# Optimization experiments

Measured on AMD Instinct MI355X. Metric: run time of the kernel, lower is better.

The kernel has to match this reference:

```python
import jax, jax.numpy as jnp
import numpy as np

B, S, D = 1, 4096, 2048
H = 16
HD = D // H  # 128
BASE = 10000.0


def setup_inputs() -> dict:
    key = jax.random.key(0)
    ks = jax.random.split(key, 6)
    hidden_states = jax.random.normal(ks[0], (B, S, D), dtype=jnp.float32)
    position_ids = jnp.broadcast_to(jnp.arange(S, dtype=jnp.int64 if jax.config.jax_enable_x64 else jnp.int32), (B, S))
    scale = 1.0 / np.sqrt(D)
    Wq = jax.random.normal(ks[1], (D, D), dtype=jnp.float32) * scale
    Wk = jax.random.normal(ks[2], (D, D), dtype=jnp.float32) * scale
    Wv = jax.random.normal(ks[3], (D, D), dtype=jnp.float32) * scale
    Wo = jax.random.normal(ks[4], (D, D), dtype=jnp.float32) * scale
    return {"hidden_states": hidden_states, "Wq": Wq, "Wk": Wk, "Wv": Wv, "Wo": Wo, "position_ids": position_ids}


def _rotate_half(x):
    x1, x2 = x[..., : x.shape[-1] // 2], x[..., x.shape[-1] // 2 :]
    return jnp.concatenate((-x2, x1), axis=-1)


def reference(hidden_states, Wq, Wk, Wv, Wo, position_ids):
    # QKV projections (torch Linear: x @ W.T)
    q = hidden_states @ Wq.T  # [B,S,D]
    k = hidden_states @ Wk.T
    v = hidden_states @ Wv.T
    # split heads -> [B,H,S,HD]
    q = q.reshape(B, S, H, HD).transpose(0, 2, 1, 3)
    k = k.reshape(B, S, H, HD).transpose(0, 2, 1, 3)
    v = v.reshape(B, S, H, HD).transpose(0, 2, 1, 3)
    # RoPE tables over seq positions
    inv_freq = 1.0 / (BASE ** (jnp.arange(0, HD, 2, dtype=jnp.float32) / HD))  # [HD/2]
    t = jnp.arange(S, dtype=jnp.float32)
    freqs = t[:, None] * inv_freq[None, :]            # [S, HD/2]
    emb = jnp.concatenate((freqs, freqs), axis=-1)    # [S, HD]
    cos = jnp.cos(emb)[position_ids][:, None]         # [B,1,S,HD]
    sin = jnp.sin(emb)[position_ids][:, None]
    q = q * cos + _rotate_half(q) * sin
    k = k * cos + _rotate_half(k) * sin
    # attention (num_kv_heads == num_heads, so no GQA repeat)
    scores = jnp.einsum("bhqd,bhkd->bhqk", q, k) / jnp.sqrt(jnp.float32(HD))
    attn = jax.nn.softmax(scores, axis=-1)
    out = jnp.einsum("bhqk,bhkd->bhqd", attn, v)      # [B,H,S,HD]
    out = out.transpose(0, 2, 1, 3).reshape(B, S, D)
    return out @ Wo.T
```

## Files before the change

kernel.cpp:

```cpp
#include <hip/hip_runtime.h>
#include <hip/hip_bf16.h>

#define S_LEN 4096
#define DMODEL 2048
#define NHEADS 16
#define HEADDIM 128
#define LDQ 6144

typedef __attribute__((ext_vector_type(8))) short bf16x8;
typedef __attribute__((ext_vector_type(4))) float f32x4;

__device__ __forceinline__ float bf2f(ushort u) {
  union { unsigned int i; float f; } x; x.i = ((unsigned int)u) << 16; return x.f;
}
__device__ __forceinline__ ushort f2bf(float f) {
  union { float f; unsigned int i; } x; x.f = f;
  unsigned int u = x.i;
  unsigned int r = u + 0x7fffu + ((u >> 16) & 1u);
  return (ushort)(r >> 16);
}
__device__ __forceinline__ unsigned int cvtpk(float a, float b) {
  unsigned int r;
  asm("v_cvt_pk_bf16_f32 %0, %1, %2" : "=v"(r) : "v"(a), "v"(b));
  return r;
}
__device__ __forceinline__ float fexp2(float x) {
  float r;
  asm("v_exp_f32 %0, %1" : "=v"(r) : "v"(x));
  return r;
}

__device__ __forceinline__ void gload16(const ushort* g, ushort* l) {
  __builtin_amdgcn_global_load_lds(
      (const __attribute__((address_space(1))) unsigned int*)g,
      (__attribute__((address_space(3))) unsigned int*)l, 16, 0, 0);
}

__global__ __launch_bounds__(256) void rope_table_kernel(float* __restrict__ cosT,
                                                         float* __restrict__ sinT) {
  int idx = blockIdx.x * 256 + threadIdx.x;
  int t = idx >> 6, j = idx & 63;
  float expo = (float)(2 * j) / 128.0f;
  float inv = 1.0f / powf(10000.0f, expo);
  float f = (float)t * inv;
  cosT[idx] = cosf(f);
  sinT[idx] = sinf(f);
}

__global__ __launch_bounds__(256) void convert_kernel(const float* __restrict__ in,
                                                      ushort* __restrict__ hi) {
  int i = (blockIdx.x * 256 + threadIdx.x) * 4;
  float4 v = *reinterpret_cast<const float4*>(&in[i]);
  ushort4 h;
  h.x = f2bf(v.x); h.y = f2bf(v.y); h.z = f2bf(v.z); h.w = f2bf(v.w);
  *reinterpret_cast<ushort4*>(&hi[i]) = h;
}

__global__ __launch_bounds__(256) void prep_weights(const float* __restrict__ Wq,
                                                    const float* __restrict__ Wk,
                                                    const float* __restrict__ Wv,
                                                    const float* __restrict__ Wo,
                                                    ushort* __restrict__ Wqkv,
                                                    ushort* __restrict__ Woh) {
  int i = (blockIdx.x * 256 + threadIdx.x) * 4;
  int which = blockIdx.y;
  const float* src = (which == 0) ? Wq : (which == 1) ? Wk : (which == 2) ? Wv : Wo;
  ushort* dst = (which == 3) ? Woh : (Wqkv + (size_t)which * DMODEL * DMODEL);
  float4 v = *reinterpret_cast<const float4*>(&src[i]);
  ushort4 h;
  h.x = f2bf(v.x); h.y = f2bf(v.y); h.z = f2bf(v.z); h.w = f2bf(v.w);
  *reinterpret_cast<ushort4*>(&dst[i]) = h;
}

__global__ __launch_bounds__(256) void gemm_qkv(const ushort* __restrict__ Ah_,
                                                const ushort* __restrict__ Bh_,
                                                ushort* __restrict__ Cout,
                                                int M, int N, int K) {
  __shared__ __align__(16) ushort sAh[128 * 64], sBh[128 * 64];
  const int tid = threadIdx.x;
  const int wave = tid >> 6, lane = tid & 63;
  const int lg = lane >> 4, lm = lane & 15;
  const int nwg = gridDim.x * gridDim.y;
  const int id = blockIdx.y * gridDim.x + blockIdx.x;
  const int cpx = nwg >> 3;
  const int swz = (id & 7) * cpx + (id >> 3);
  const int nbx = N >> 7;
  const int m0 = (swz / nbx) * 128, n0 = (swz % nbx) * 128;
  const int wm = (wave >> 1) * 64, wn = (wave & 1) * 64;
  f32x4 acc[4][4] = {};

  int srow[4], scc[4], lbs[4];
#pragma unroll
  for (int it = 0; it < 4; ++it) {
    int ci = it * 256 + wave * 64 + lane;
    srow[it] = ci >> 3;
    scc[it] = (ci & 7) ^ (srow[it] & 7);
    lbs[it] = (it * 256 + wave * 64) * 8;
  }

  for (int k0 = 0; k0 < K; k0 += 64) {
    __syncthreads();
#pragma unroll
    for (int it = 0; it < 4; ++it) {
      size_t ga = (size_t)(m0 + srow[it]) * K + k0 + scc[it] * 8;
      size_t gb = (size_t)(n0 + srow[it]) * K + k0 + scc[it] * 8;
      gload16(&Ah_[ga], &sAh[lbs[it]]);
      gload16(&Bh_[gb], &sBh[lbs[it]]);
    }
    __syncthreads();
    bf16x8 ah[4][2], bh[4][2];
#pragma unroll
    for (int t = 0; t < 4; ++t)
#pragma unroll
      for (int kc = 0; kc < 2; ++kc) {
        int Ra = wm + t * 16 + lm;
        int Rb = wn + t * 16 + lm;
        int pa_ = ((kc * 4 + lg) ^ (Ra & 7)) * 8;
        int pb_ = ((kc * 4 + lg) ^ (Rb & 7)) * 8;
        ah[t][kc] = *reinterpret_cast<const bf16x8*>(&sAh[Ra * 64 + pa_]);
        bh[t][kc] = *reinterpret_cast<const bf16x8*>(&sBh[Rb * 64 + pb_]);
      }
#pragma unroll
    for (int kc = 0; kc < 2; ++kc)
#pragma unroll
      for (int mi = 0; mi < 4; ++mi)
#pragma unroll
        for (int ni = 0; ni < 4; ++ni)
          acc[mi][ni] = __builtin_amdgcn_mfma_f32_16x16x32_bf16(ah[mi][kc], bh[ni][kc], acc[mi][ni], 0, 0, 0);
  }
#pragma unroll
  for (int mi = 0; mi < 4; ++mi)
#pragma unroll
    for (int ni = 0; ni < 4; ++ni)
#pragma unroll
      for (int j = 0; j < 4; ++j) {
        int row = m0 + wm + mi * 16 + lg * 4 + j;
        int col = n0 + wn + ni * 16 + lm;
        Cout[(size_t)row * N + col] = f2bf(acc[mi][ni][j]);
      }
}

__global__ __launch_bounds__(256) void gemm1o64(const ushort* __restrict__ Ah_,
                                                const ushort* __restrict__ Bh_,
                                                float* __restrict__ Cout,
                                                int M, int N, int K) {
  __shared__ __align__(16) ushort sAh[128 * 64], sBh[128 * 64];
  const int tid = threadIdx.x;
  const int wave = tid >> 6, lane = tid & 63;
  const int lg = lane >> 4, lm = lane & 15;
  const int nwg = gridDim.x * gridDim.y;
  const int id = blockIdx.y * gridDim.x + blockIdx.x;
  const int cpx = nwg >> 3;
  const int swz = (id & 7) * cpx + (id >> 3);
  const int nbx = N >> 7;
  const int m0 = (swz / nbx) * 128, n0 = (swz % nbx) * 128;
  const int wm = (wave >> 1) * 64, wn = (wave & 1) * 64;
  f32x4 acc[4][4] = {};

  int srow[4], scc[4], lbs[4];
#pragma unroll
  for (int it = 0; it < 4; ++it) {
    int ci = it * 256 + wave * 64 + lane;
    srow[it] = ci >> 3;
    scc[it] = (ci & 7) ^ (srow[it] & 7);
    lbs[it] = (it * 256 + wave * 64) * 8;
  }

  for (int k0 = 0; k0 < K; k0 += 64) {
    __syncthreads();
#pragma unroll
    for (int it = 0; it < 4; ++it) {
      size_t ga = (size_t)(m0 + srow[it]) * K + k0 + scc[it] * 8;
      size_t gb = (size_t)(n0 + srow[it]) * K + k0 + scc[it] * 8;
      gload16(&Ah_[ga], &sAh[lbs[it]]);
      gload16(&Bh_[gb], &sBh[lbs[it]]);
    }
    __syncthreads();
    bf16x8 ah[4][2], bh[4][2];
#pragma unroll
    for (int t = 0; t < 4; ++t)
#pragma unroll
      for (int kc = 0; kc < 2; ++kc) {
        int Ra = wm + t * 16 + lm;
        int Rb = wn + t * 16 + lm;
        int pa_ = ((kc * 4 + lg) ^ (Ra & 7)) * 8;
        int pb_ = ((kc * 4 + lg) ^ (Rb & 7)) * 8;
        ah[t][kc] = *reinterpret_cast<const bf16x8*>(&sAh[Ra * 64 + pa_]);
        bh[t][kc] = *reinterpret_cast<const bf16x8*>(&sBh[Rb * 64 + pb_]);
      }
#pragma unroll
    for (int kc = 0; kc < 2; ++kc)
#pragma unroll
      for (int mi = 0; mi < 4; ++mi)
#pragma unroll
        for (int ni = 0; ni < 4; ++ni)
          acc[mi][ni] = __builtin_amdgcn_mfma_f32_16x16x32_bf16(ah[mi][kc], bh[ni][kc], acc[mi][ni], 0, 0, 0);
  }
#pragma unroll
  for (int mi = 0; mi < 4; ++mi)
#pragma unroll
    for (int ni = 0; ni < 4; ++ni)
#pragma unroll
      for (int j = 0; j < 4; ++j) {
        int row = m0 + wm + mi * 16 + lg * 4 + j;
        int col = n0 + wn + ni * 16 + lm;
        Cout[(size_t)row * N + col] = acc[mi][ni][j];
      }
}

__global__ __launch_bounds__(256) void rope2_kernel(ushort* __restrict__ QKV,
                                                    const int* __restrict__ pos,
                                                    const float* __restrict__ cosT,
                                                    const float* __restrict__ sinT) {
  int t = blockIdx.x * 256 + threadIdx.x;
  int j0 = (t & 7) * 8;
  int hh = (t >> 3) & 15;
  int s = t >> 7;
  int p = pos[s];
  float cs[8], sn[8];
  *reinterpret_cast<float4*>(&cs[0]) = *reinterpret_cast<const float4*>(&cosT[p * 64 + j0]);
  *reinterpret_cast<float4*>(&cs[4]) = *reinterpret_cast<const float4*>(&cosT[p * 64 + j0 + 4]);
  *reinterpret_cast<float4*>(&sn[0]) = *reinterpret_cast<const float4*>(&sinT[p * 64 + j0]);
  *reinterpret_cast<float4*>(&sn[4]) = *reinterpret_cast<const float4*>(&sinT[p * 64 + j0 + 4]);
  size_t base = (size_t)s * LDQ + hh * HEADDIM + j0;
  union u8 { uint4 v; ushort e[8]; };
  u8 qa, qb, ka, kb;
  qa.v = *reinterpret_cast<const uint4*>(&QKV[base]);
  qb.v = *reinterpret_cast<const uint4*>(&QKV[base + 64]);
  ka.v = *reinterpret_cast<const uint4*>(&QKV[base + DMODEL]);
  kb.v = *reinterpret_cast<const uint4*>(&QKV[base + DMODEL + 64]);
  const float scl = 0.12751742f;
#pragma unroll
  for (int e = 0; e < 8; ++e) {
    float q1 = bf2f(qa.e[e]), q2 = bf2f(qb.e[e]);
    float k1 = bf2f(ka.e[e]), k2 = bf2f(kb.e[e]);
    qa.e[e] = f2bf((q1 * cs[e] - q2 * sn[e]) * scl);
    qb.e[e] = f2bf((q2 * cs[e] + q1 * sn[e]) * scl);
    ka.e[e] = f2bf(k1 * cs[e] - k2 * sn[e]);
    kb.e[e] = f2bf(k2 * cs[e] + k1 * sn[e]);
  }
  *reinterpret_cast<uint4*>(&QKV[base]) = qa.v;
  *reinterpret_cast<uint4*>(&QKV[base + 64]) = qb.v;
  *reinterpret_cast<uint4*>(&QKV[base + DMODEL]) = ka.v;
  *reinterpret_cast<uint4*>(&QKV[base + DMODEL + 64]) = kb.v;
}

__global__ __launch_bounds__(256) void transpose_kernel(const ushort* __restrict__ Vr,
                                                        ushort* __restrict__ Vt) {
  __shared__ __align__(16) ushort tile[64 * 72];
  int tid = threadIdx.x;
  int s0 = blockIdx.x * 64, c0 = blockIdx.y * 64;
#pragma unroll
  for (int it = 0; it < 2; ++it) {
    int i = tid + it * 256;
    int r = i >> 3, c = i & 7;
    *reinterpret_cast<uint4*>(&tile[r * 72 + c * 8]) =
        *reinterpret_cast<const uint4*>(&Vr[(size_t)(s0 + r) * LDQ + c0 + c * 8]);
  }
  __syncthreads();
#pragma unroll
  for (int it = 0; it < 2; ++it) {
    int i = tid + it * 256;
    int cr = i >> 3, sc = i & 7;
    ushort tmp[8];
#pragma unroll
    for (int j = 0; j < 8; ++j) tmp[j] = tile[(sc * 8 + j) * 72 + cr];
    *reinterpret_cast<uint4*>(&Vt[(size_t)(c0 + cr) * S_LEN + s0 + sc * 8]) =
        *reinterpret_cast<uint4*>(tmp);
  }
}

#define FTILE(STC, STN, VCUR, KWB, VWB, KRB, T)                                           \
  {                                                                                       \
    float m16[2];                                                                         \
    _Pragma("unroll") for (int t2 = 0; t2 < 2; ++t2) {                                    \
      float m = fmaxf(STC[t2][0][0], STC[t2][0][1]);                                      \
      m = fmaxf(fmaxf(m, STC[t2][0][2]), STC[t2][0][3]);                                  \
      m = fmaxf(fmaxf(m, STC[t2][1][0]), STC[t2][1][1]);                                  \
      m = fmaxf(fmaxf(m, STC[t2][1][2]), STC[t2][1][3]);                                  \
      m = fmaxf(fmaxf(m, STC[t2][2][0]), STC[t2][2][1]);                                  \
      m = fmaxf(fmaxf(m, STC[t2][2][2]), STC[t2][2][3]);                                  \
      m = fmaxf(fmaxf(m, STC[t2][3][0]), STC[t2][3][1]);                                  \
      m = fmaxf(fmaxf(m, STC[t2][3][2]), STC[t2][3][3]);                                  \
      m = fmaxf(m, __shfl_xor(m, 16));                                                    \
      m = fmaxf(m, __shfl_xor(m, 32));                                                    \
      m16[t2] = m;                                                                        \
    }                                                                                     \
    bool grow = (m16[0] > mrun[0] + 11.5f) || (m16[1] > mrun[1] + 11.5f);                 \
    if (__any(grow)) {                                                                    \
      _Pragma("unroll") for (int t2 = 0; t2 < 2; ++t2) {                                  \
        float mn = fmaxf(mrun[t2], m16[t2]);                                              \
        float scl = fexp2(mrun[t2] - mn);                                                 \
        mrun[t2] = mn;                                                                    \
        float sj[4];                                                                      \
        _Pragma("unroll") for (int j = 0; j < 4; ++j) sj[j] = __shfl(scl, lg * 4 + j);    \
        _Pragma("unroll") for (int j = 0; j < 4; ++j) osum[t2][j] *= sj[j];               \
        _Pragma("unroll") for (int nb = 0; nb < 8; ++nb)                                  \
            _Pragma("unroll") for (int j = 0; j < 4; ++j) oacc[t2][nb][j] *= sj[j];       \
      }                                                                                   \
    }                                                                                     \
    _Pragma("unroll") for (int t2 = 0; t2 < 2; ++t2)                                      \
        _Pragma("unroll") for (int nf = 0; nf < 4; ++nf)                                  \
            _Pragma("unroll") for (int j = 0; j < 4; ++j)                                 \
                STC[t2][nf][j] = fexp2(STC[t2][nf][j] - mrun[t2]);                        \
    bf16x8 pa[2][2];                                                                      \
    _Pragma("unroll") for (int t2 = 0; t2 < 2; ++t2)                                      \
        _Pragma("unroll") for (int kk = 0; kk < 2; ++kk) {                                \
      union { unsigned int u[4]; bf16x8 v; } w_;                                          \
      w_.u[0] = cvtpk(STC[t2][kk][0], STC[t2][kk][1]);                                    \
      w_.u[1] = cvtpk(STC[t2][kk][2], STC[t2][kk][3]);                                    \
      w_.u[2] = cvtpk(STC[t2][2 + kk][0], STC[t2][2 + kk][1]);                            \
      w_.u[3] = cvtpk(STC[t2][2 + kk][2], STC[t2][2 + kk][3]);                            \
      pa[t2][kk] = w_.v;                                                                  \
    }                                                                                     \
    __builtin_amdgcn_s_setprio(1);                                                        \
    _Pragma("unroll") for (int t2 = 0; t2 < 2; ++t2) {                                    \
      osum[t2] = __builtin_amdgcn_mfma_f32_16x16x32_bf16(pa[t2][0], ones, osum[t2], 0, 0, 0); \
      osum[t2] = __builtin_amdgcn_mfma_f32_16x16x32_bf16(pa[t2][1], ones, osum[t2], 0, 0, 0); \
    }                                                                                     \
    _Pragma("unroll") for (int nb = 0; nb < 8; ++nb)                                      \
        _Pragma("unroll") for (int kk = 0; kk < 2; ++kk) {                                \
      int pc = (kk * 4 + lg) ^ (lm & 7);                                                  \
      bf16x8 vfrag = *reinterpret_cast<const bf16x8*>(&VCUR[(nb * 16 + lm) * 64 + pc * 8]); \
      oacc[0][nb] = __builtin_amdgcn_mfma_f32_16x16x32_bf16(pa[0][kk], vfrag, oacc[0][nb], 0, 0, 0); \
      oacc[1][nb] = __builtin_amdgcn_mfma_f32_16x16x32_bf16(pa[1][kk], vfrag, oacc[1][nb], 0, 0, 0); \
    }                                                                                     \
    __builtin_amdgcn_s_setprio(0);                                                        \
    __syncthreads();                                                                      \
    if ((T) + 2 < 64) {                                                                   \
      const size_t ko_ = (size_t)((T) + 2) * 64;                                          \
      _Pragma("unroll") for (int k = 0; k < 4; ++k) {                                     \
        gload16(pK[k] + ko_ * LDQ, &KWB[lbs[k]]);                                         \
        gload16(pV[k] + ko_, &VWB[lbs[k]]);                                               \
      }                                                                                   \
    }                                                                                     \
    if ((T) + 1 < 64) {                                                                   \
      _Pragma("unroll") for (int t2 = 0; t2 < 2; ++t2)                                    \
          _Pragma("unroll") for (int nf = 0; nf < 4; ++nf) STN[t2][nf] = fzero;           \
      __builtin_amdgcn_s_setprio(1);                                                      \
      _Pragma("unroll") for (int nf = 0; nf < 4; ++nf)                                    \
          _Pragma("unroll") for (int kc = 0; kc < 4; ++kc) {                              \
        int pc = (kc * 4 + lg) ^ (lm & 7);                                                \
        bf16x8 kfrag = *reinterpret_cast<const bf16x8*>(&KRB[(nf * 16 + lm) * 128 + pc * 8]); \
        STN[0][nf] = __builtin_amdgcn_mfma_f32_16x16x32_bf16(kfrag, qh[0][kc], STN[0][nf], 0, 0, 0); \
        STN[1][nf] = __builtin_amdgcn_mfma_f32_16x16x32_bf16(kfrag, qh[1][kc], STN[1][nf], 0, 0, 0); \
      }                                                                                   \
      __builtin_amdgcn_s_setprio(0);                                                      \
    }                                                                                     \
  }

__global__ __launch_bounds__(256, 2) void flash14_kernel(const ushort* __restrict__ QKV,
                                                         const ushort* __restrict__ Vt,
                                                         ushort* __restrict__ Oh) {
  __shared__ __align__(16) ushort KtA[64 * 128];
  __shared__ __align__(16) ushort KtB[64 * 128];
  __shared__ __align__(16) ushort VsA[128 * 64];
  __shared__ __align__(16) ushort VsB[128 * 64];
  const int tid = threadIdx.x;
  const int wave = tid >> 6, lane = tid & 63;
  const int lg = lane >> 4, lm = lane & 15;
  const int id = blockIdx.y * gridDim.x + blockIdx.x;
  const int o = (id & 7) * 64 + (id >> 3);
  const int h = o >> 5;
  const int q0 = (o & 31) * 128;
  const f32x4 fzero = {};

  bf16x8 qh[2][4];
#pragma unroll
  for (int t2 = 0; t2 < 2; ++t2) {
    int qrow = q0 + wave * 32 + t2 * 16 + lm;
#pragma unroll
    for (int kc = 0; kc < 4; ++kc)
      qh[t2][kc] = *reinterpret_cast<const bf16x8*>(
          &QKV[(size_t)qrow * LDQ + h * HEADDIM + kc * 32 + lg * 8]);
  }

  bf16x8 ones;
#pragma unroll
  for (int i = 0; i < 8; ++i) ones[i] = (short)0x3f80;

  auto rho = [](int s) {
    return 32 * ((s >> 4) & 1) + 8 * ((s >> 2) & 3) + 4 * (s >> 5) + (s & 3);
  };
  const ushort* Kb = QKV + DMODEL;
  const ushort* pK[4];
  const ushort* pV[4];
  int lbs[4];
#pragma unroll
  for (int k = 0; k < 4; ++k) {
    int ci = k * 256 + wave * 64 + lane;
    int ks = ci >> 4;
    int kcc = (ci & 15) ^ (ks & 7);
    pK[k] = Kb + (size_t)rho(ks) * LDQ + h * HEADDIM + kcc * 8;
    int vd = ci >> 3;
    int vcc = (ci & 7) ^ (vd & 7);
    pV[k] = Vt + (size_t)(h * HEADDIM + vd) * S_LEN + vcc * 8;
    lbs[k] = (k * 256 + wave * 64) * 8;
  }

  f32x4 oacc[2][8] = {};
  f32x4 osum[2] = {};
  float mrun[2];
#pragma unroll
  for (int t2 = 0; t2 < 2; ++t2) mrun[t2] = -3.0e38f;

#pragma unroll
  for (int k = 0; k < 4; ++k) {
    gload16(pK[k], &KtA[lbs[k]]);
    gload16(pV[k], &VsA[lbs[k]]);
  }
  __syncthreads();
#pragma unroll
  for (int k = 0; k < 4; ++k) {
    gload16(pK[k] + (size_t)64 * LDQ, &KtB[lbs[k]]);
    gload16(pV[k] + 64, &VsB[lbs[k]]);
  }
  f32x4 stA[2][4], stB[2][4];
#pragma unroll
  for (int t2 = 0; t2 < 2; ++t2)
#pragma unroll
    for (int nf = 0; nf < 4; ++nf) stA[t2][nf] = fzero;
  __builtin_amdgcn_s_setprio(1);
#pragma unroll
  for (int nf = 0; nf < 4; ++nf)
#pragma unroll
    for (int kc = 0; kc < 4; ++kc) {
      int pc = (kc * 4 + lg) ^ (lm & 7);
      bf16x8 kfrag = *reinterpret_cast<const bf16x8*>(&KtA[(nf * 16 + lm) * 128 + pc * 8]);
      stA[0][nf] = __builtin_amdgcn_mfma_f32_16x16x32_bf16(kfrag, qh[0][kc], stA[0][nf], 0, 0, 0);
      stA[1][nf] = __builtin_amdgcn_mfma_f32_16x16x32_bf16(kfrag, qh[1][kc], stA[1][nf], 0, 0, 0);
    }
  __builtin_amdgcn_s_setprio(0);

  for (int tp = 0; tp < 32; ++tp) {
    const int t0 = 2 * tp;
    FTILE(stA, stB, VsA, KtA, VsA, KtB, t0)
    FTILE(stB, stA, VsB, KtB, VsB, KtA, t0 + 1)
  }

#pragma unroll
  for (int t2 = 0; t2 < 2; ++t2) {
    float linv[4];
#pragma unroll
    for (int j = 0; j < 4; ++j) linv[j] = 1.0f / osum[t2][j];
#pragma unroll
    for (int nb = 0; nb < 8; ++nb)
#pragma unroll
      for (int j = 0; j < 4; ++j) {
        int row = q0 + wave * 32 + t2 * 16 + lg * 4 + j;
        int col = h * HEADDIM + nb * 16 + lm;
        Oh[(size_t)row * DMODEL + col] = f2bf(oacc[t2][nb][j] * linv[j]);
      }
  }
}

extern "C" void kernel_launch(void* const* d_in, const int* in_sizes, int n_in,
                              void* d_out, int out_size, void* d_ws, size_t ws_size,
                              hipStream_t stream) {
  (void)in_sizes; (void)n_in; (void)out_size; (void)ws_size;
  const float* X  = (const float*)d_in[0];
  const float* Wq = (const float*)d_in[1];
  const float* Wk = (const float*)d_in[2];
  const float* Wv = (const float*)d_in[3];
  const float* Wo = (const float*)d_in[4];
  const int* pos  = (const int*)d_in[5];
  float* out = (float*)d_out;

  ushort* wb = (ushort*)d_ws;
  const size_t SD = (size_t)S_LEN * DMODEL;
  const size_t DD = (size_t)DMODEL * DMODEL;

  ushort* Xh   = wb;
  ushort* QKV  = wb + 2 * SD;
  ushort* Vt   = wb + 5 * SD;
  ushort* W0h  = wb + 6 * SD;
  ushort* Wqkv = wb + 7 * SD;
  float* cosT  = (float*)(wb + 9 * SD);
  float* sinT  = cosT + (size_t)S_LEN * 64;
  ushort* OhB  = Wqkv;

  rope_table_kernel<<<S_LEN * 64 / 256, 256, 0, stream>>>(cosT, sinT);
  convert_kernel<<<SD / 1024, 256, 0, stream>>>(X, Xh);
  prep_weights<<<dim3(DD / 1024, 4), 256, 0, stream>>>(Wq, Wk, Wv, Wo, Wqkv, W0h);

  gemm_qkv<<<dim3(LDQ / 128, S_LEN / 128), 256, 0, stream>>>(Xh, Wqkv, QKV, S_LEN, LDQ, DMODEL);

  rope2_kernel<<<(S_LEN * 1024 / 8) / 256, 256, 0, stream>>>(QKV, pos, cosT, sinT);
  transpose_kernel<<<dim3(S_LEN / 64, DMODEL / 64), 256, 0, stream>>>(QKV + 2 * DMODEL, Vt);

  flash14_kernel<<<dim3(32, 16), 256, 0, stream>>>(QKV, Vt, OhB);

  dim3 gemmGrid(DMODEL / 128, S_LEN / 128);
  gemm1o64<<<gemmGrid, 256, 0, stream>>>(OhB, W0h, out, S_LEN, DMODEL, DMODEL);
}
```

Before: 339.9 us.

## Software-pipeline flash attention QK^T one tile ahead; fuse prep kernels

Restructures the flash attention loop so each iteration computes QK^T for the next K tile before running softmax and PV on the previous scores. This lets the MFMA work overlap with the exp/softmax VALU work, and K and V loads are now issued on separate schedules into their buffers. The three preprocessing kernels (rope table, X conversion, weight conversion) are also merged into one launch with a 7-row grid to cut launch overhead. The cost is more live registers for the two score tiles and more intricate buffer-reuse timing.

```diff
diff --git a/kernel.cpp b/kernel.cpp
--- a/kernel.cpp
+++ b/kernel.cpp
@@ -36,40 +36,41 @@
       (__attribute__((address_space(3))) unsigned int*)l, 16, 0, 0);
 }
 
-__global__ __launch_bounds__(256) void rope_table_kernel(float* __restrict__ cosT,
-                                                         float* __restrict__ sinT) {
-  int idx = blockIdx.x * 256 + threadIdx.x;
-  int t = idx >> 6, j = idx & 63;
-  float expo = (float)(2 * j) / 128.0f;
-  float inv = 1.0f / powf(10000.0f, expo);
-  float f = (float)t * inv;
-  cosT[idx] = cosf(f);
-  sinT[idx] = sinf(f);
-}
-
-__global__ __launch_bounds__(256) void convert_kernel(const float* __restrict__ in,
-                                                      ushort* __restrict__ hi) {
-  int i = (blockIdx.x * 256 + threadIdx.x) * 4;
-  float4 v = *reinterpret_cast<const float4*>(&in[i]);
-  ushort4 h;
-  h.x = f2bf(v.x); h.y = f2bf(v.y); h.z = f2bf(v.z); h.w = f2bf(v.w);
-  *reinterpret_cast<ushort4*>(&hi[i]) = h;
-}
-
-__global__ __launch_bounds__(256) void prep_weights(const float* __restrict__ Wq,
-                                                    const float* __restrict__ Wk,
-                                                    const float* __restrict__ Wv,
-                                                    const float* __restrict__ Wo,
-                                                    ushort* __restrict__ Wqkv,
-                                                    ushort* __restrict__ Woh) {
-  int i = (blockIdx.x * 256 + threadIdx.x) * 4;
+__global__ __launch_bounds__(256) void prep_all(const float* __restrict__ X,
+                                                const float* __restrict__ Wq,
+                                                const float* __restrict__ Wk,
+                                                const float* __restrict__ Wv,
+                                                const float* __restrict__ Wo,
+                                                ushort* __restrict__ Xh,
+                                                ushort* __restrict__ Wqkv,
+                                                ushort* __restrict__ Woh,
+                                                float* __restrict__ cosT,
+                                                float* __restrict__ sinT) {
   int which = blockIdx.y;
-  const float* src = (which == 0) ? Wq : (which == 1) ? Wk : (which == 2) ? Wv : Wo;
-  ushort* dst = (which == 3) ? Woh : (Wqkv + (size_t)which * DMODEL * DMODEL);
-  float4 v = *reinterpret_cast<const float4*>(&src[i]);
-  ushort4 h;
-  h.x = f2bf(v.x); h.y = f2bf(v.y); h.z = f2bf(v.z); h.w = f2bf(v.w);
-  *reinterpret_cast<ushort4*>(&dst[i]) = h;
+  if (which < 4) {
+    int i = (blockIdx.x * 256 + threadIdx.x) * 4;
+    const float* src = (which == 0) ? Wq : (which == 1) ? Wk : (which == 2) ? Wv : Wo;
+    ushort* dst = (which == 3) ? Woh : (Wqkv + (size_t)which * DMODEL * DMODEL);
+    float4 v = *reinterpret_cast<const float4*>(&src[i]);
+    ushort4 h;
+    h.x = f2bf(v.x); h.y = f2bf(v.y); h.z = f2bf(v.z); h.w = f2bf(v.w);
+    *reinterpret_cast<ushort4*>(&dst[i]) = h;
+  } else if (which < 6) {
+    int i = (((which - 4) * 4096 + blockIdx.x) * 256 + threadIdx.x) * 4;
+    float4 v = *reinterpret_cast<const float4*>(&X[i]);
+    ushort4 h;
+    h.x = f2bf(v.x); h.y = f2bf(v.y); h.z = f2bf(v.z); h.w = f2bf(v.w);
+    *reinterpret_cast<ushort4*>(&Xh[i]) = h;
+  } else {
+    if (blockIdx.x >= 1024) return;
+    int idx = blockIdx.x * 256 + threadIdx.x;
+    int t = idx >> 6, j = idx & 63;
+    float expo = (float)(2 * j) / 128.0f;
+    float inv = 1.0f / powf(10000.0f, expo);
+    float f = (float)t * inv;
+    cosT[idx] = cosf(f);
+    sinT[idx] = sinf(f);
+  }
 }
 
 __global__ __launch_bounds__(256) void gemm_qkv(const ushort* __restrict__ Ah_,
@@ -270,18 +271,34 @@
   }
 }
 
-#define FTILE(STC, STN, VCUR, KWB, VWB, KRB, T)                                           \
+
+#define QKT15(STC, KRD)                                                                   \
+  {                                                                                       \
+    _Pragma("unroll") for (int t2 = 0; t2 < 2; ++t2)                                      \
+        _Pragma("unroll") for (int nf = 0; nf < 4; ++nf) STC[t2][nf] = fzero;             \
+    __builtin_amdgcn_s_setprio(1);                                                        \
+    _Pragma("unroll") for (int nf = 0; nf < 4; ++nf)                                      \
+        _Pragma("unroll") for (int kc = 0; kc < 4; ++kc) {                                \
+      int pc = (kc * 4 + lg) ^ (lm & 7);                                                  \
+      bf16x8 kfrag = *reinterpret_cast<const bf16x8*>(&KRD[(nf * 16 + lm) * 128 + pc * 8]); \
+      STC[0][nf] = __builtin_amdgcn_mfma_f32_16x16x32_bf16(kfrag, qh[0][kc], STC[0][nf], 0, 0, 0); \
+      STC[1][nf] = __builtin_amdgcn_mfma_f32_16x16x32_bf16(kfrag, qh[1][kc], STC[1][nf], 0, 0, 0); \
+    }                                                                                     \
+    __builtin_amdgcn_s_setprio(0);                                                        \
+  }
+
+#define SMPV15(STP, VPR)                                                                  \
   {                                                                                       \
     float m16[2];                                                                         \
     _Pragma("unroll") for (int t2 = 0; t2 < 2; ++t2) {                                    \
-      float m = fmaxf(STC[t2][0][0], STC[t2][0][1]);                                      \
-      m = fmaxf(fmaxf(m, STC[t2][0][2]), STC[t2][0][3]);                                  \
-      m = fmaxf(fmaxf(m, STC[t2][1][0]), STC[t2][1][1]);                                  \
-      m = fmaxf(fmaxf(m, STC[t2][1][2]), STC[t2][1][3]);                                  \
-      m = fmaxf(fmaxf(m, STC[t2][2][0]), STC[t2][2][1]);                                  \
-      m = fmaxf(fmaxf(m, STC[t2][2][2]), STC[t2][2][3]);                                  \
-      m = fmaxf(fmaxf(m, STC[t2][3][0]), STC[t2][3][1]);                                  \
-      m = fmaxf(fmaxf(m, STC[t2][3][2]), STC[t2][3][3]);                                  \
+      float m = fmaxf(STP[t2][0][0], STP[t2][0][1]);                                      \
+      m = fmaxf(fmaxf(m, STP[t2][0][2]), STP[t2][0][3]);                                  \
+      m = fmaxf(fmaxf(m, STP[t2][1][0]), STP[t2][1][1]);                                  \
+      m = fmaxf(fmaxf(m, STP[t2][1][2]), STP[t2][1][3]);                                  \
+      m = fmaxf(fmaxf(m, STP[t2][2][0]), STP[t2][2][1]);                                  \
+      m = fmaxf(fmaxf(m, STP[t2][2][2]), STP[t2][2][3]);                                  \
+      m = fmaxf(fmaxf(m, STP[t2][3][0]), STP[t2][3][1]);                                  \
+      m = fmaxf(fmaxf(m, STP[t2][3][2]), STP[t2][3][3]);                                  \
       m = fmaxf(m, __shfl_xor(m, 16));                                                    \
       m = fmaxf(m, __shfl_xor(m, 32));                                                    \
       m16[t2] = m;                                                                        \
@@ -302,15 +319,15 @@
     _Pragma("unroll") for (int t2 = 0; t2 < 2; ++t2)                                      \
         _Pragma("unroll") for (int nf = 0; nf < 4; ++nf)                                  \
             _Pragma("unroll") for (int j = 0; j < 4; ++j)                                 \
-                STC[t2][nf][j] = fexp2(STC[t2][nf][j] - mrun[t2]);                        \
+                STP[t2][nf][j] = fexp2(STP[t2][nf][j] - mrun[t2]);                        \
     bf16x8 pa[2][2];                                                                      \
     _Pragma("unroll") for (int t2 = 0; t2 < 2; ++t2)                                      \
         _Pragma("unroll") for (int kk = 0; kk < 2; ++kk) {                                \
       union { unsigned int u[4]; bf16x8 v; } w_;                                          \
-      w_.u[0] = cvtpk(STC[t2][kk][0], STC[t2][kk][1]);                                    \
-      w_.u[1] = cvtpk(STC[t2][kk][2], STC[t2][kk][3]);                                    \
-      w_.u[2] = cvtpk(STC[t2][2 + kk][0], STC[t2][2 + kk][1]);                            \
-      w_.u[3] = cvtpk(STC[t2][2 + kk][2], STC[t2][2 + kk][3]);                            \
+      w_.u[0] = cvtpk(STP[t2][kk][0], STP[t2][kk][1]);                                    \
+      w_.u[1] = cvtpk(STP[t2][kk][2], STP[t2][kk][3]);                                    \
+      w_.u[2] = cvtpk(STP[t2][2 + kk][0], STP[t2][2 + kk][1]);                            \
+      w_.u[3] = cvtpk(STP[t2][2 + kk][2], STP[t2][2 + kk][3]);                            \
       pa[t2][kk] = w_.v;                                                                  \
     }                                                                                     \
     __builtin_amdgcn_s_setprio(1);                                                        \
@@ -321,35 +338,29 @@
     _Pragma("unroll") for (int nb = 0; nb < 8; ++nb)                                      \
         _Pragma("unroll") for (int kk = 0; kk < 2; ++kk) {                                \
       int pc = (kk * 4 + lg) ^ (lm & 7);                                                  \
-      bf16x8 vfrag = *reinterpret_cast<const bf16x8*>(&VCUR[(nb * 16 + lm) * 64 + pc * 8]); \
+      bf16x8 vfrag = *reinterpret_cast<const bf16x8*>(&VPR[(nb * 16 + lm) * 64 + pc * 8]); \
       oacc[0][nb] = __builtin_amdgcn_mfma_f32_16x16x32_bf16(pa[0][kk], vfrag, oacc[0][nb], 0, 0, 0); \
       oacc[1][nb] = __builtin_amdgcn_mfma_f32_16x16x32_bf16(pa[1][kk], vfrag, oacc[1][nb], 0, 0, 0); \
     }                                                                                     \
     __builtin_amdgcn_s_setprio(0);                                                        \
+  }
+
+#define BODY15(STC, STP, KRD, VPR, T)                                                     \
+  {                                                                                       \
+    QKT15(STC, KRD)                                                                       \
+    SMPV15(STP, VPR)                                                                      \
     __syncthreads();                                                                      \
     if ((T) + 2 < 64) {                                                                   \
       const size_t ko_ = (size_t)((T) + 2) * 64;                                          \
-      _Pragma("unroll") for (int k = 0; k < 4; ++k) {                                     \
-        gload16(pK[k] + ko_ * LDQ, &KWB[lbs[k]]);                                         \
-        gload16(pV[k] + ko_, &VWB[lbs[k]]);                                               \
-      }                                                                                   \
+      _Pragma("unroll") for (int k = 0; k < 4; ++k) gload16(pK[k] + ko_ * LDQ, &KRD[lbs[k]]); \
     }                                                                                     \
     if ((T) + 1 < 64) {                                                                   \
-      _Pragma("unroll") for (int t2 = 0; t2 < 2; ++t2)                                    \
-          _Pragma("unroll") for (int nf = 0; nf < 4; ++nf) STN[t2][nf] = fzero;           \
-      __builtin_amdgcn_s_setprio(1);                                                      \
-      _Pragma("unroll") for (int nf = 0; nf < 4; ++nf)                                    \
-          _Pragma("unroll") for (int kc = 0; kc < 4; ++kc) {                              \
-        int pc = (kc * 4 + lg) ^ (lm & 7);                                                \
-        bf16x8 kfrag = *reinterpret_cast<const bf16x8*>(&KRB[(nf * 16 + lm) * 128 + pc * 8]); \
-        STN[0][nf] = __builtin_amdgcn_mfma_f32_16x16x32_bf16(kfrag, qh[0][kc], STN[0][nf], 0, 0, 0); \
-        STN[1][nf] = __builtin_amdgcn_mfma_f32_16x16x32_bf16(kfrag, qh[1][kc], STN[1][nf], 0, 0, 0); \
-      }                                                                                   \
-      __builtin_amdgcn_s_setprio(0);                                                      \
-    }                                                                                     \
-  }
-
-__global__ __launch_bounds__(256, 2) void flash14_kernel(const ushort* __restrict__ QKV,
+      const size_t vo_ = (size_t)((T) + 1) * 64;                                          \
+      _Pragma("unroll") for (int k = 0; k < 4; ++k) gload16(pV[k] + vo_, &VPR[lbs[k]]);   \
+    }                                                                                     \
+  }
+
+__global__ __launch_bounds__(256, 2) void flash15_kernel(const ushort* __restrict__ QKV,
                                                          const ushort* __restrict__ Vt,
                                                          ushort* __restrict__ Oh) {
   __shared__ __align__(16) ushort KtA[64 * 128];
@@ -404,6 +415,8 @@
 #pragma unroll
   for (int t2 = 0; t2 < 2; ++t2) mrun[t2] = -3.0e38f;
 
+  f32x4 stA[2][4], stB[2][4];
+
 #pragma unroll
   for (int k = 0; k < 4; ++k) {
     gload16(pK[k], &KtA[lbs[k]]);
@@ -411,32 +424,24 @@
   }
   __syncthreads();
 #pragma unroll
+  for (int k = 0; k < 4; ++k) gload16(pK[k] + (size_t)64 * LDQ, &KtB[lbs[k]]);
+
+  QKT15(stA, KtA)
+  __syncthreads();
+#pragma unroll
   for (int k = 0; k < 4; ++k) {
-    gload16(pK[k] + (size_t)64 * LDQ, &KtB[lbs[k]]);
+    gload16(pK[k] + (size_t)128 * LDQ, &KtA[lbs[k]]);
     gload16(pV[k] + 64, &VsB[lbs[k]]);
   }
-  f32x4 stA[2][4], stB[2][4];
-#pragma unroll
-  for (int t2 = 0; t2 < 2; ++t2)
-#pragma unroll
-    for (int nf = 0; nf < 4; ++nf) stA[t2][nf] = fzero;
-  __builtin_amdgcn_s_setprio(1);
-#pragma unroll
-  for (int nf = 0; nf < 4; ++nf)
-#pragma unroll
-    for (int kc = 0; kc < 4; ++kc) {
-      int pc = (kc * 4 + lg) ^ (lm & 7);
-      bf16x8 kfrag = *reinterpret_cast<const bf16x8*>(&KtA[(nf * 16 + lm) * 128 + pc * 8]);
-      stA[0][nf] = __builtin_amdgcn_mfma_f32_16x16x32_bf16(kfrag, qh[0][kc], stA[0][nf], 0, 0, 0);
-      stA[1][nf] = __builtin_amdgcn_mfma_f32_16x16x32_bf16(kfrag, qh[1][kc], stA[1][nf], 0, 0, 0);
-    }
-  __builtin_amdgcn_s_setprio(0);
-
-  for (int tp = 0; tp < 32; ++tp) {
-    const int t0 = 2 * tp;
-    FTILE(stA, stB, VsA, KtA, VsA, KtB, t0)
-    FTILE(stB, stA, VsB, KtB, VsB, KtA, t0 + 1)
-  }
+
+  for (int tp = 0; tp < 31; ++tp) {
+    const int t1 = 2 * tp + 1;
+    BODY15(stB, stA, KtB, VsA, t1)
+    BODY15(stA, stB, KtA, VsB, t1 + 1)
+  }
+  BODY15(stB, stA, KtB, VsA, 63)
+
+  SMPV15(stB, VsB)
 
 #pragma unroll
   for (int t2 = 0; t2 < 2; ++t2) {
@@ -479,16 +484,14 @@
   float* sinT  = cosT + (size_t)S_LEN * 64;
   ushort* OhB  = Wqkv;
 
-  rope_table_kernel<<<S_LEN * 64 / 256, 256, 0, stream>>>(cosT, sinT);
-  convert_kernel<<<SD / 1024, 256, 0, stream>>>(X, Xh);
-  prep_weights<<<dim3(DD / 1024, 4), 256, 0, stream>>>(Wq, Wk, Wv, Wo, Wqkv, W0h);
+  prep_all<<<dim3(DD / 1024, 7), 256, 0, stream>>>(X, Wq, Wk, Wv, Wo, Xh, Wqkv, W0h, cosT, sinT);
 
   gemm_qkv<<<dim3(LDQ / 128, S_LEN / 128), 256, 0, stream>>>(Xh, Wqkv, QKV, S_LEN, LDQ, DMODEL);
 
   rope2_kernel<<<(S_LEN * 1024 / 8) / 256, 256, 0, stream>>>(QKV, pos, cosT, sinT);
   transpose_kernel<<<dim3(S_LEN / 64, DMODEL / 64), 256, 0, stream>>>(QKV + 2 * DMODEL, Vt);
 
-  flash14_kernel<<<dim3(32, 16), 256, 0, stream>>>(QKV, Vt, OhB);
+  flash15_kernel<<<dim3(32, 16), 256, 0, stream>>>(QKV, Vt, OhB);
 
   dim3 gemmGrid(DMODEL / 128, S_LEN / 128);
   gemm1o64<<<gemmGrid, 256, 0, stream>>>(OhB, W0h, out, S_LEN, DMODEL, DMODEL);
```

After: 335.2 us. No clear change (-1.4%).
